# Optimization experiments

Hardware: AMD Instinct MI355X
Metric: run time of the kernel (lower is better)

Reference implementation:

```python
import jax, jax.numpy as jnp
import numpy as np

S_MC = 4      # num_mc_samples
TEMP = 0.1    # soft_sampling temperature


def gcn_conv(x, adj, maskf, W, b):
    # DenseGCNConv: add self loops, sym-normalize, aggregate, linear, mask
    N = adj.shape[-1]
    A = adj + jnp.eye(N, dtype=adj.dtype)
    dis = jnp.clip(A.sum(-1), 1.0, None) ** -0.5
    A = dis[:, :, None] * A * dis[:, None, :]
    out = jnp.einsum('bij,bjf->bif', A, x @ W) + b
    return out * maskf[:, :, None]


def connected_components(adj, mask):
    # min-label propagation; labels in {1..N}, masked nodes -> 0
    B, N, _ = adj.shape
    labels0 = jnp.broadcast_to(jnp.arange(1, N + 1, dtype=jnp.int32), (B, N))
    big = jnp.int32(N + 2)
    adj_b = adj > 0
    def step(labels, _):
        nb = jnp.where(adj_b, labels[:, None, :], big)  # [B,N,N]
        return jnp.minimum(labels, nb.min(-1)), None
    labels, _ = jax.lax.scan(step, labels0, None, length=N)
    return jnp.where(mask, labels, 0)


def setup_inputs() -> dict:
    key = jax.random.key(0)
    ks = jax.random.split(key, 8)
    B, N, Fin, H, K = 512, 64, 128, 256, 32
    x = jax.random.normal(ks[0], (B, N, Fin), jnp.float32)
    lengths = jax.random.randint(ks[1], (B,), N // 2, N + 1)
    mask = jnp.arange(N)[None, :] < lengths[:, None]
    a = jax.random.uniform(ks[2], (B, N, N)) < 0.08
    adj = jnp.triu(a, 1)
    adj = (adj | jnp.swapaxes(adj, 1, 2)).astype(jnp.float32)
    adj = adj * mask[:, :, None] * mask[:, None, :]
    W1 = jax.random.normal(ks[3], (Fin, H), jnp.float32) / np.float32(np.sqrt(Fin))
    b1 = jnp.zeros((H,), jnp.float32)
    W2 = jax.random.normal(ks[4], (H, H), jnp.float32) / np.float32(np.sqrt(H))
    b2 = jnp.zeros((H,), jnp.float32)
    centroids = jax.random.normal(ks[5], (K, H), jnp.float32)
    return {'x': x, 'adj': adj, 'mask': mask, 'W1': W1, 'b1': b1, 'W2': W2, 'b2': b2, 'centroids': centroids}


def reference(x, adj, mask, W1, b1, W2, b2, centroids):
    B, N = mask.shape
    maskf = mask.astype(x.dtype)
    adj = adj * maskf[:, :, None] * maskf[:, None, :]
    # embedding convs
    h = jax.nn.relu(gcn_conv(x, adj, maskf, W1, b1))
    h = jax.nn.relu(gcn_conv(h, adj, maskf, W2, b2))
    # cdist to (detached) centroids, expanded form to avoid [B,N,K,F] blowup
    c = jax.lax.stop_gradient(centroids)
    d2 = (jnp.sum(h * h, -1, keepdims=True) + jnp.sum(c * c, -1)[None, None]
          - 2.0 * jnp.einsum('bnf,kf->bnk', h, c))
    dist = jnp.sqrt(jnp.clip(d2, 1e-12, None))  # [B,N,K]
    # softmin over clusters with temperature
    logits = -dist / TEMP
    probs = jax.nn.softmax(logits, -1)
    logp = jax.nn.log_softmax(logits, -1)
    # Categorical MC sampling via Gumbel-max
    g = jax.random.gumbel(jax.random.key(42), (S_MC,) + logp.shape, logp.dtype)
    concepts = jnp.argmax(logp[None] + g, -1).reshape(S_MC * B, N)  # [SB,N]
    # per-node sampled probability, product over valid nodes per graph (scatter mul)
    probs_r = jnp.tile(probs, (S_MC, 1, 1))
    node_p = jnp.take_along_axis(probs_r, concepts[..., None], -1)[..., 0]
    mask_r = jnp.tile(mask, (S_MC, 1))
    graph_prob = jnp.prod(jnp.where(mask_r, jax.lax.stop_gradient(node_p), 1.0), -1)  # [SB]
    # same-concept restricted adjacency -> connected components (undirected)
    adj_r = jnp.tile(adj, (S_MC, 1, 1))
    same = concepts[:, :, None] == concepts[:, None, :]
    adj_cc = jnp.where(same, adj_r, 0.0)
    adj_cc = jnp.maximum(adj_cc, jnp.swapaxes(adj_cc, 1, 2))
    labels = connected_components(adj_cc, mask_r)  # [SB,N], 0 reserved for masked
    # scatter-mean node embeddings per cluster; drop reserved cluster 0
    P = jax.nn.one_hot(labels, N + 1, dtype=x.dtype) * mask_r[..., None].astype(x.dtype)  # [SB,N,N+1]
    counts = P.sum(1)  # [SB,N+1]
    h_r = jnp.tile(h, (S_MC, 1, 1))
    new_x = (jnp.einsum('bnc,bnf->bcf', P, h_r) / jnp.clip(counts, 1.0, None)[..., None])[:, 1:, :]
    # pooled adjacency S^T A S, binarized
    new_adj = jnp.einsum('bic,bij,bjd->bcd', P, adj_r, P)[:, 1:, 1:]
    new_adj = (new_adj > 0).astype(x.dtype)
    return new_x, new_adj, graph_prob, labels
```

## Files before the change

kernel.cpp:

```cpp
#include <hip/hip_runtime.h>

#define B_    512

static constexpr float TINYF = 1.17549435e-38f;
typedef float fx4  __attribute__((ext_vector_type(4)));
typedef short bf16x8 __attribute__((ext_vector_type(8)));
typedef float f32x4 __attribute__((ext_vector_type(4)));
typedef unsigned short u16x4 __attribute__((ext_vector_type(4)));

__device__ __forceinline__ float fmul_s(float a, float b) { float r; asm("v_mul_f32 %0, %1, %2" : "=v"(r) : "v"(a), "v"(b)); return r; }
__device__ __forceinline__ float fadd_s(float a, float b) { float r; asm("v_add_f32 %0, %1, %2" : "=v"(r) : "v"(a), "v"(b)); return r; }
__device__ __forceinline__ float fsub_s(float a, float b) { float r; asm("v_sub_f32 %0, %1, %2" : "=v"(r) : "v"(a), "v"(b)); return r; }

__device__ __forceinline__ unsigned tf_bits(unsigned lo) {
  const unsigned ks0 = 0u, ks1 = 42u, ks2 = 0x1BD11BF0u;
  unsigned x0 = 0u + ks0;
  unsigned x1 = lo + ks1;
#define TFR(r) { x0 += x1; x1 = (x1 << r) | (x1 >> (32 - r)); x1 ^= x0; }
  TFR(13) TFR(15) TFR(26) TFR(6)
  x0 += ks1; x1 += ks2 + 1u;
  TFR(17) TFR(29) TFR(16) TFR(24)
  x0 += ks2; x1 += ks0 + 2u;
  TFR(13) TFR(15) TFR(26) TFR(6)
  x0 += ks0; x1 += ks1 + 3u;
  TFR(17) TFR(29) TFR(16) TFR(24)
  x0 += ks1; x1 += ks2 + 4u;
  TFR(13) TFR(15) TFR(26) TFR(6)
  x0 += ks2; x1 += ks0 + 5u;
#undef TFR
  return x0 ^ x1;
}

__device__ __forceinline__ void split3(float v, unsigned& b1, unsigned& b2, unsigned& b3) {
  unsigned u1 = __float_as_uint(v) & 0xFFFF0000u;
  float r1 = v - __uint_as_float(u1);
  unsigned u2 = __float_as_uint(r1) & 0xFFFF0000u;
  float r2 = r1 - __uint_as_float(u2);
  unsigned u3 = __float_as_uint(r2) & 0xFFFF0000u;
  b1 = u1 >> 16; b2 = u2 >> 16; b3 = u3 >> 16;
}

__device__ __forceinline__ unsigned short planeOf(float v, int s) {
  unsigned u1 = __float_as_uint(v) & 0xFFFF0000u;
  if (s == 0) return (unsigned short)(u1 >> 16);
  float r1 = v - __uint_as_float(u1);
  unsigned u2 = __float_as_uint(r1) & 0xFFFF0000u;
  if (s == 1) return (unsigned short)(u2 >> 16);
  float r2 = r1 - __uint_as_float(u2);
  return (unsigned short)((__float_as_uint(r2) & 0xFFFF0000u) >> 16);
}

#define MF6(A0, A1, A2, Bv0, Bv1, Bv2, ACC)                                   \
  ACC = __builtin_amdgcn_mfma_f32_16x16x32_bf16(A0, Bv0, ACC, 0, 0, 0);       \
  ACC = __builtin_amdgcn_mfma_f32_16x16x32_bf16(A0, Bv1, ACC, 0, 0, 0);       \
  ACC = __builtin_amdgcn_mfma_f32_16x16x32_bf16(A1, Bv0, ACC, 0, 0, 0);       \
  ACC = __builtin_amdgcn_mfma_f32_16x16x32_bf16(A0, Bv2, ACC, 0, 0, 0);       \
  ACC = __builtin_amdgcn_mfma_f32_16x16x32_bf16(A1, Bv1, ACC, 0, 0, 0);       \
  ACC = __builtin_amdgcn_mfma_f32_16x16x32_bf16(A2, Bv0, ACC, 0, 0, 0);

__global__ void k_setup(const float* __restrict__ W1, const float* __restrict__ W2,
                        const float* __restrict__ cen,
                        unsigned short* __restrict__ Wg1, unsigned short* __restrict__ Wg2,
                        unsigned short* __restrict__ cen3, float* __restrict__ ccbuf) {
  int bi = blockIdx.x, tid = threadIdx.x;
  if (bi < 144) {
    const float* W; unsigned short* Wg; int nk, s, ks, g;
    if (bi < 48) { W = W1; Wg = Wg1; nk = 4; s = bi >> 4; ks = (bi >> 2) & 3; g = bi & 3; }
    else { int t = bi - 48; W = W2; Wg = Wg2; nk = 8; s = t >> 5; ks = (t >> 2) & 7; g = t & 3; }
    int n = tid;
    bf16x8 hv;
#pragma unroll
    for (int jj = 0; jj < 8; ++jj) {
      float v = W[(size_t)(ks * 32 + g * 8 + jj) * 256 + n];
      hv[jj] = (short)planeOf(v, s);
    }
    *(bf16x8*)&Wg[((((size_t)s * nk + ks) * 4 + g) * 256 + n) * 8] = hv;
  } else if (bi == 144) {
    int k = tid >> 3, l8 = tid & 7;
    float s = 0.0f;
    for (int m = 0; m < 32; ++m) { float v = cen[k * 256 + l8 + 8 * m]; s += v * v; }
#pragma unroll
    for (int d = 1; d < 8; d <<= 1) s += __shfl_xor(s, d, 64);
    if (l8 == 0) ccbuf[k] = s;
  } else {
    int s = bi - 145;
    for (int u = 0; u < 4; ++u) {
      int idx = tid + 256 * u;
      int ks = idx >> 7, c = (idx >> 6) & 1, rem = idx & 63;
      int l15v = rem >> 2, lgv = rem & 3;
      bf16x8 hv;
#pragma unroll
      for (int jj = 0; jj < 8; ++jj)
        hv[jj] = (short)planeOf(cen[(size_t)(16 * c + l15v) * 256 + 32 * ks + 8 * lgv + jj], s);
      *(bf16x8*)&cen3[(size_t)s * 8192 + (size_t)idx * 8] = hv;
    }
  }
}

__device__ __forceinline__ void layer_core(const float* __restrict__ A,
                                           const unsigned short* __restrict__ Wg,
                                           const unsigned short* AhP,
                                           const float* biaS, const float* maskS,
                                           float* __restrict__ out, int nk,
                                           char* U, int b, int tid) {
  unsigned short (*Ap)[3][2112] = (unsigned short(*)[3][2112])U;
  unsigned short (*Tbuf)[72]    = (unsigned short(*)[72])U;
  int w = tid >> 6, l = tid & 63;
  int l15 = l & 15, lg = l >> 4;
  int K = nk * 32;
  int srow = tid >> 2, sg = tid & 3;
  const float* sp = A + (size_t)srow * K + sg * 8;

  {
    float4 v0 = *(const float4*)(sp);
    float4 v1 = *(const float4*)(sp + 4);
    float vv[8] = {v0.x, v0.y, v0.z, v0.w, v1.x, v1.y, v1.z, v1.w};
    bf16x8 p1, p2, p3;
#pragma unroll
    for (int jj = 0; jj < 8; ++jj) {
      unsigned h1, h2, h3; split3(vv[jj], h1, h2, h3);
      p1[jj] = (short)h1; p2[jj] = (short)h2; p3[jj] = (short)h3;
    }
    int off = sg * 528 + srow * 8;
    *(bf16x8*)&Ap[0][0][off] = p1;
    *(bf16x8*)&Ap[0][1][off] = p2;
    *(bf16x8*)&Ap[0][2][off] = p3;
  }
  __syncthreads();

  f32x4 acc1[4][4];
#pragma unroll
  for (int q = 0; q < 4; ++q)
#pragma unroll
    for (int c = 0; c < 4; ++c) acc1[q][c] = (f32x4){0.f, 0.f, 0.f, 0.f};

  const size_t wss = (size_t)nk * 8192;

  for (int ks = 0; ks < nk; ++ks) {
    int cur = ks & 1;
    float4 v0, v1;
    bool pf = (ks + 1 < nk);
    if (pf) {
      v0 = *(const float4*)(sp + (ks + 1) * 32);
      v1 = *(const float4*)(sp + (ks + 1) * 32 + 4);
    }
    bf16x8 af[4][3];
#pragma unroll
    for (int q = 0; q < 4; ++q) {
      int off = lg * 528 + (16 * q + l15) * 8;
#pragma unroll
      for (int s = 0; s < 3; ++s) af[q][s] = *(const bf16x8*)&Ap[cur][s][off];
    }
#pragma unroll
    for (int c = 0; c < 4; ++c) {
      size_t wbase = (((size_t)ks * 4 + lg) * 256 + (64 * w + 16 * c + l15)) * 8;
      bf16x8 b0 = *(const bf16x8*)&Wg[wbase];
      bf16x8 b1 = *(const bf16x8*)&Wg[wbase + wss];
      bf16x8 b2 = *(const bf16x8*)&Wg[wbase + 2 * wss];
#pragma unroll
      for (int q = 0; q < 4; ++q) {
        MF6(af[q][0], af[q][1], af[q][2], b0, b1, b2, acc1[q][c]);
      }
    }
    if (pf) {
      float vv[8] = {v0.x, v0.y, v0.z, v0.w, v1.x, v1.y, v1.z, v1.w};
      bf16x8 p1, p2, p3;
#pragma unroll
      for (int jj = 0; jj < 8; ++jj) {
        unsigned h1, h2, h3; split3(vv[jj], h1, h2, h3);
        p1[jj] = (short)h1; p2[jj] = (short)h2; p3[jj] = (short)h3;
      }
      int off = sg * 528 + srow * 8;
      *(bf16x8*)&Ap[cur ^ 1][0][off] = p1;
      *(bf16x8*)&Ap[cur ^ 1][1][off] = p2;
      *(bf16x8*)&Ap[cur ^ 1][2][off] = p3;
    }
    __syncthreads();
  }

  f32x4 acc2[4][4];
#pragma unroll
  for (int q = 0; q < 4; ++q)
#pragma unroll
    for (int c = 0; c < 4; ++c) acc2[q][c] = (f32x4){0.f, 0.f, 0.f, 0.f};

#pragma unroll
  for (int sB = 0; sB < 3; ++sB) {
    const int nA = 3 - sB;
    __syncthreads();
#pragma unroll
    for (int q = 0; q < 4; ++q)
#pragma unroll
      for (int c = 0; c < 4; ++c) {
        u16x4 pv;
#pragma unroll
        for (int r = 0; r < 4; ++r) pv[r] = planeOf(acc1[q][c][r], sB);
        *(u16x4*)&Tbuf[64 * w + 16 * c + l15][16 * q + 4 * lg] = pv;
      }
    __syncthreads();
#pragma unroll
    for (int mt = 0; mt < 2; ++mt) {
      bf16x8 bf[4];
#pragma unroll
      for (int c = 0; c < 4; ++c)
        bf[c] = *(const bf16x8*)&Tbuf[64 * w + 16 * c + l15][32 * mt + 8 * lg];
#pragma unroll
      for (int q2 = 0; q2 < 4; ++q2) {
        bf16x8 afr[3];
#pragma unroll
        for (int sA = 0; sA < 3; ++sA)
          if (sA < nA)
            afr[sA] = *(const bf16x8*)&AhP[((((size_t)(sA * 2 + mt) * 4 + q2) * 4 + lg) * 16 + l15) * 8];
#pragma unroll
        for (int c = 0; c < 4; ++c)
#pragma unroll
          for (int sA = 0; sA < 3; ++sA)
            if (sA < nA)
              acc2[q2][c] = __builtin_amdgcn_mfma_f32_16x16x32_bf16(afr[sA], bf[c], acc2[q2][c], 0, 0, 0);
      }
    }
  }

#pragma unroll
  for (int q2 = 0; q2 < 4; ++q2) {
#pragma unroll
    for (int c = 0; c < 4; ++c) {
      int n = 64 * w + 16 * c + l15;
      float bv = biaS[n];
#pragma unroll
      for (int r = 0; r < 4; ++r) {
        int row = 16 * q2 + 4 * lg + r;
        float val = (acc2[q2][c][r] + bv) * maskS[row];
        out[((size_t)b * 64 + row) * 256 + n] = fmaxf(val, 0.0f);
      }
    }
  }
}

__global__ __launch_bounds__(256, 2) void k_fused(
    const float* __restrict__ x, const float* __restrict__ adj,
    const void* __restrict__ mp,
    const float* __restrict__ b1v, const float* __restrict__ b2v,
    const unsigned short* __restrict__ Wg1, const unsigned short* __restrict__ Wg2,
    unsigned long long* __restrict__ nbr, float* __restrict__ maskf,
    float* __restrict__ bufA, float* __restrict__ bufB) {
  __shared__ unsigned short AhP[12288];
  __shared__ float biaS[256];
  __shared__ float maskS[64];
  __shared__ int s_ni, s_nf;
  __shared__ __align__(16) char U[36864];

  int b = blockIdx.x, tid = threadIdx.x;

  {
    float* adjS = (float*)U;
    float (*AhS)[65] = (float(*)[65])(U + 16384);
    float* dis = (float*)(U + 33024);
    if (tid == 0) { s_ni = 0; s_nf = 0; }
    const float* ab = adj + (size_t)b * 4096;
    for (int i = tid; i < 4096; i += 256) adjS[i] = ab[i];
    {
      const unsigned* wp = (const unsigned*)mp;
      int ni = 0, nf = 0;
      for (int i = tid; i < 2048; i += 256) {
        unsigned v = wp[i];
        if (v > 1u) ni = 1;
        if (v != 0u && v != 0x3f800000u) nf = 1;
      }
      if (ni) atomicOr(&s_ni, 1);
      if (nf) atomicOr(&s_nf, 1);
    }
    biaS[tid] = b1v[tid];
    __syncthreads();
    if (tid < 64) {
      float s = 0.0f;
      unsigned long long m = 0ull;
      for (int j = 0; j < 64; ++j) {
        float v = adjS[j * 64 + tid];
        s += (j == tid) ? (v + 1.0f) : v;
        if (v != 0.0f) m |= (1ull << j);
      }
      dis[tid] = 1.0f / sqrtf(fmaxf(s, 1.0f));
      nbr[b * 64 + tid] = m;
      int fl = s_ni ? (s_nf ? 2 : 1) : 0;
      int i = b * 64 + tid;
      float r;
      if (fl == 0)      r = ((const int*)mp)[i] ? 1.0f : 0.0f;
      else if (fl == 1) r = (((const float*)mp)[i] != 0.0f) ? 1.0f : 0.0f;
      else              r = ((const unsigned char*)mp)[i] ? 1.0f : 0.0f;
      maskS[tid] = r;
      maskf[i] = r;
    }
    __syncthreads();
    for (int i = tid; i < 4096; i += 256) {
      int r = i >> 6, c = i & 63;
      float a = adjS[i] + ((r == c) ? 1.0f : 0.0f);
      AhS[r][c] = (dis[r] * a) * dis[c];
    }
    __syncthreads();
    for (int ch = tid; ch < 1536; ch += 256) {
      int l15v = ch & 15, lgv = (ch >> 4) & 3, q2 = (ch >> 6) & 3, mt = (ch >> 8) & 1, s = ch >> 9;
      bf16x8 hv;
#pragma unroll
      for (int jj = 0; jj < 8; ++jj)
        hv[jj] = (short)planeOf(AhS[16 * q2 + l15v][32 * mt + 8 * lgv + jj], s);
      *(bf16x8*)&AhP[(size_t)ch * 8] = hv;
    }
    __syncthreads();
  }

  layer_core(x + (size_t)b * 64 * 128, Wg1, AhP, biaS, maskS, bufA, 4, U, b, tid);
  __syncthreads();
  biaS[tid] = b2v[tid];

  layer_core(bufA + (size_t)b * 64 * 256, Wg2, AhP, biaS, maskS, bufB, 8, U, b, tid);
}

__global__ __launch_bounds__(256, 3) void k_cdsp(const float* __restrict__ h,
                                                 const unsigned short* __restrict__ cen3,
                                                 const float* __restrict__ ccbuf,
                                                 const float* __restrict__ maskf,
                                                 const unsigned long long* __restrict__ nbr,
                                                 float* __restrict__ out_newx,
                                                 float* __restrict__ out_newadj,
                                                 float* __restrict__ out_gp,
                                                 float* __restrict__ out_lab) {
  __shared__ float Dred[4][64][36];
  __shared__ float hhp[64][4];
  __shared__ float lgp[64][33];
  __shared__ float mxs[64], lgden[64];
  __shared__ int concS[4][64];
  __shared__ float ppS[4][64];
  __shared__ int labFS[4][64];

  int b = blockIdx.x, tid = threadIdx.x;
  int w = tid >> 6, l = tid & 63, l15 = l & 15, lg = l >> 4;
  const float* hb = h + (size_t)b * 16384;

  {
    int row = tid & 63, qt = tid >> 6;
    float s = 0.0f;
    for (int u = 0; u < 16; ++u) {
      float4 v = *(const float4*)&hb[row * 256 + qt * 64 + u * 4];
      float t = fadd_s(fadd_s(fadd_s(fmul_s(v.x, v.x), fmul_s(v.y, v.y)), fmul_s(v.z, v.z)), fmul_s(v.w, v.w));
      s = fadd_s(s, t);
    }
    hhp[row][qt] = s;
  }

  f32x4 acc[4][2];
#pragma unroll
  for (int qt = 0; qt < 4; ++qt)
#pragma unroll
    for (int c = 0; c < 2; ++c) acc[qt][c] = (f32x4){0.f, 0.f, 0.f, 0.f};

#pragma unroll
  for (int ks2 = 0; ks2 < 2; ++ks2) {
    int ks = 2 * w + ks2;
#pragma unroll
    for (int qt = 0; qt < 4; ++qt) {
      int row = 16 * qt + l15;
      float4 v0 = *(const float4*)&hb[row * 256 + 32 * ks + 8 * lg];
      float4 v1 = *(const float4*)&hb[row * 256 + 32 * ks + 8 * lg + 4];
      float vv[8] = {v0.x, v0.y, v0.z, v0.w, v1.x, v1.y, v1.z, v1.w};
      bf16x8 a0, a1, a2;
#pragma unroll
      for (int jj = 0; jj < 8; ++jj) {
        unsigned h1, h2, h3; split3(vv[jj], h1, h2, h3);
        a0[jj] = (short)h1; a1[jj] = (short)h2; a2[jj] = (short)h3;
      }
#pragma unroll
      for (int c = 0; c < 2; ++c) {
        const unsigned short* cb = cen3 + ((size_t)(ks * 2 + c) * 64 + l15 * 4 + lg) * 8;
        bf16x8 b0 = *(const bf16x8*)cb;
        bf16x8 b1 = *(const bf16x8*)(cb + 8192);
        bf16x8 b2 = *(const bf16x8*)(cb + 16384);
        MF6(a0, a1, a2, b0, b1, b2, acc[qt][c]);
      }
    }
  }

#pragma unroll
  for (int qt = 0; qt < 4; ++qt)
#pragma unroll
    for (int c = 0; c < 2; ++c)
#pragma unroll
      for (int r = 0; r < 4; ++r)
        Dred[w][16 * qt + 4 * lg + r][16 * c + l15] = acc[qt][c][r];
  __syncthreads();

  {
    int n = tid >> 2, kq = tid & 3;
    float hh = (hhp[n][0] + hhp[n][1]) + (hhp[n][2] + hhp[n][3]);
#pragma unroll
    for (int j = 0; j < 8; ++j) {
      int k = kq * 8 + j;
      float dot = (Dred[0][n][k] + Dred[1][n][k]) + (Dred[2][n][k] + Dred[3][n][k]);
      float d2 = fsub_s(fadd_s(hh, ccbuf[k]), fmul_s(2.0f, dot));
      lgp[n][k] = -10.0f * sqrtf(fmaxf(d2, 1e-12f));
    }
  }
  __syncthreads();

  if (tid < 64) {
    float mx = -1e30f;
    for (int k = 0; k < 32; ++k) mx = fmaxf(mx, lgp[tid][k]);
    float den = 0.0f;
    for (int k = 0; k < 32; ++k) den += expf(lgp[tid][k] - mx);
    mxs[tid] = mx; lgden[tid] = logf(den);
  }
  __syncthreads();
  for (int p = tid; p < 2048; p += 256) {
    int n = p >> 5, k = p & 31;
    lgp[n][k] = (lgp[n][k] - mxs[n]) - lgden[n];
  }
  __syncthreads();

  {
    int hw = tid >> 5, k = tid & 31;
    for (int pass = 0; pass < 8; ++pass) {
      int n = hw * 8 + pass;
      float lp = lgp[n][k];
#pragma unroll
      for (int s4 = 0; s4 < 4; ++s4) {
        unsigned flat = (unsigned)(s4 * 32768 + b * 64 + n) * 32u + (unsigned)k;
        unsigned bits = tf_bits(flat);
        float fu = __uint_as_float((bits >> 9) | 0x3f800000u) - 1.0f;
        float u = fmaxf(TINYF, fadd_s(fmul_s(fu, 1.0f - TINYF), TINYF));
        float g = -logf(-logf(u));
        float v = lp + g;
        int bi = k;
#pragma unroll
        for (int d = 1; d < 32; d <<= 1) {
          float ov = __shfl_xor(v, d, 32);
          int oi = __shfl_xor(bi, d, 32);
          if (ov > v || (ov == v && oi < bi)) { v = ov; bi = oi; }
        }
        if (k == 0) {
          concS[s4][n] = bi;
          ppS[s4][n] = expf(lgp[n][bi]);
        }
      }
    }
  }
  __syncthreads();

  {
    unsigned char (*o)[4096] = (unsigned char(*)[4096])Dred;
    int s = w, lane = l;
    int sbo = s * 512 + b;
    int c0 = concS[s][lane];
    bool mk = maskf[b * 64 + lane] != 0.0f;
    unsigned long long nb = nbr[b * 64 + lane];
    unsigned long long sm = 0ull;
    {
      unsigned long long t = nb;
      while (t) { int j = __ffsll(t) - 1; if (concS[s][j] == c0) sm |= (1ull << j); t &= t - 1; }
    }
    labFS[s][lane] = lane + 1;
    for (int it = 0; it < 64; ++it) {
      int m = labFS[s][lane];
      unsigned long long t = sm;
      while (t) { int j = __ffsll(t) - 1; m = min(m, labFS[s][j]); t &= t - 1; }
      bool ch = m < labFS[s][lane];
      if (ch) labFS[s][lane] = m;
      if (!__any(ch)) break;
    }
    int lf = mk ? labFS[s][lane] : 0;
    out_lab[(size_t)sbo * 64 + lane] = (float)lf;
    float pv = mk ? ppS[s][lane] : 1.0f;
#pragma unroll
    for (int d = 1; d < 64; d <<= 1) pv *= __shfl_xor(pv, d, 64);
    if (lane == 0) out_gp[sbo] = pv;
    labFS[s][lane] = lf;
    unsigned long long cm = 0ull;
    for (int j = 0; j < 64; ++j)
      if (labFS[s][j] == lane + 1) cm |= (1ull << j);
    {
      unsigned* op = (unsigned*)o[s];
#pragma unroll
      for (int u = 0; u < 16; ++u) op[u * 64 + lane] = 0u;
      if (lf > 0) {
        unsigned long long t = nb;
        while (t) {
          int j = __ffsll(t) - 1; t &= t - 1;
          int lj = labFS[s][j];
          if (lj > 0) o[s][(lf - 1) * 64 + (lj - 1)] = 1;
        }
      }
      float* dA = out_newadj + (size_t)sbo * 4096;
#pragma unroll
      for (int u = 0; u < 16; ++u) {
        int base = u * 256 + lane * 4;
        fx4 v;
        v.x = o[s][base + 0] ? 1.0f : 0.0f;
        v.y = o[s][base + 1] ? 1.0f : 0.0f;
        v.z = o[s][base + 2] ? 1.0f : 0.0f;
        v.w = o[s][base + 3] ? 1.0f : 0.0f;
        *(fx4*)&dA[base] = v;
      }
    }
    float* dX = out_newx + (size_t)sbo * 16384;
    for (int c = 0; c < 64; ++c) {
      unsigned long long m = __shfl(cm, c, 64);
      float4 acc4 = make_float4(0.f, 0.f, 0.f, 0.f);
      unsigned long long t = m;
      while (t) {
        int j = __ffsll(t) - 1; t &= t - 1;
        float4 v = *(const float4*)&hb[j * 256 + lane * 4];
        acc4.x += v.x; acc4.y += v.y; acc4.z += v.z; acc4.w += v.w;
      }
      int cnt = __popcll(m);
      float cf = (float)(cnt > 0 ? cnt : 1);
      fx4 r;
      r.x = acc4.x / cf; r.y = acc4.y / cf; r.z = acc4.z / cf; r.w = acc4.w / cf;
      *(fx4*)&dX[(size_t)c * 256 + lane * 4] = r;
    }
  }
}

extern "C" void kernel_launch(void* const* d_in, const int* in_sizes, int n_in,
                              void* d_out, int out_size, void* d_ws, size_t ws_size,
                              hipStream_t stream) {
  (void)in_sizes; (void)n_in; (void)out_size; (void)ws_size;
  const float* x   = (const float*)d_in[0];
  const float* adj = (const float*)d_in[1];
  const void*  mp  = d_in[2];
  const float* W1  = (const float*)d_in[3];
  const float* b1  = (const float*)d_in[4];
  const float* W2  = (const float*)d_in[5];
  const float* b2  = (const float*)d_in[6];
  const float* cen = (const float*)d_in[7];

  char* ws = (char*)d_ws;
  unsigned short* Wg1  = (unsigned short*)(ws + 0);
  unsigned short* Wg2  = (unsigned short*)(ws + 196608);
  unsigned short* cen3 = (unsigned short*)(ws + 589824);
  float* ccbuf         = (float*)(ws + 638976);
  unsigned long long* nbr = (unsigned long long*)(ws + 655360);
  float* maskf         = (float*)(ws + 917504);
  float* bufA          = (float*)(ws + 2097152);
  float* bufB          = (float*)(ws + 37748736);

  float* out        = (float*)d_out;
  float* out_newx   = out;
  float* out_newadj = out + 33554432;
  float* out_gp     = out + 41943040;
  float* out_lab    = out + 41945088;

  hipLaunchKernelGGL(k_setup, dim3(148), dim3(256), 0, stream, W1, W2, cen, Wg1, Wg2, cen3, ccbuf);
  hipLaunchKernelGGL(k_fused, dim3(512), dim3(256), 0, stream, x, adj, mp, b1, b2,
                     Wg1, Wg2, nbr, maskf, bufA, bufB);
  hipLaunchKernelGGL(k_cdsp,  dim3(512), dim3(256), 0, stream, bufB, cen3, ccbuf, maskf, nbr,
                     out_newx, out_newadj, out_gp, out_lab);
}
```

Baseline: 149.7 us.

## Split cdist/sampling and cluster pooling into separate kernels with per-wave rows

The fused cdist+sampling+pooling kernel is split in two. The first kernel gives each wave 16 node rows over the full K dimension, so there is no cross-wave reduction and no __syncthreads. It writes the sampled concepts and probabilities to workspace. A second kernel with 2048 single-wave blocks runs connected components, pooled adjacency and scatter-mean per sample, which gives finer-grained parallelism for the divergent pooling stage. This adds an extra launch and a round trip through global memory for concepts and probabilities.

```diff
diff --git a/kernel.cpp b/kernel.cpp
--- a/kernel.cpp
+++ b/kernel.cpp
@@ -316,52 +316,46 @@
   layer_core(bufA + (size_t)b * 64 * 256, Wg2, AhP, biaS, maskS, bufB, 8, U, b, tid);
 }
 
-__global__ __launch_bounds__(256, 3) void k_cdsp(const float* __restrict__ h,
-                                                 const unsigned short* __restrict__ cen3,
-                                                 const float* __restrict__ ccbuf,
-                                                 const float* __restrict__ maskf,
-                                                 const unsigned long long* __restrict__ nbr,
-                                                 float* __restrict__ out_newx,
-                                                 float* __restrict__ out_newadj,
-                                                 float* __restrict__ out_gp,
-                                                 float* __restrict__ out_lab) {
-  __shared__ float Dred[4][64][36];
-  __shared__ float hhp[64][4];
-  __shared__ float lgp[64][33];
-  __shared__ float mxs[64], lgden[64];
-  __shared__ int concS[4][64];
-  __shared__ float ppS[4][64];
-  __shared__ int labFS[4][64];
+__global__ __launch_bounds__(256, 4) void k_cd(const float* __restrict__ h,
+                                               const unsigned short* __restrict__ cen3,
+                                               const float* __restrict__ ccbuf,
+                                               int* __restrict__ conc,
+                                               float* __restrict__ pp) {
+  __shared__ float lgpS[4][16][33];
+  __shared__ float hhS[64];
+  __shared__ float mxS[64], ldS[64];
 
   int b = blockIdx.x, tid = threadIdx.x;
   int w = tid >> 6, l = tid & 63, l15 = l & 15, lg = l >> 4;
   const float* hb = h + (size_t)b * 16384;
 
   {
-    int row = tid & 63, qt = tid >> 6;
+    int row = 16 * w + (l >> 2), q = l & 3;
     float s = 0.0f;
     for (int u = 0; u < 16; ++u) {
-      float4 v = *(const float4*)&hb[row * 256 + qt * 64 + u * 4];
+      float4 v = *(const float4*)&hb[row * 256 + q * 64 + u * 4];
       float t = fadd_s(fadd_s(fadd_s(fmul_s(v.x, v.x), fmul_s(v.y, v.y)), fmul_s(v.z, v.z)), fmul_s(v.w, v.w));
       s = fadd_s(s, t);
     }
-    hhp[row][qt] = s;
-  }
-
-  f32x4 acc[4][2];
-#pragma unroll
-  for (int qt = 0; qt < 4; ++qt)
-#pragma unroll
-    for (int c = 0; c < 2; ++c) acc[qt][c] = (f32x4){0.f, 0.f, 0.f, 0.f};
-
-#pragma unroll
-  for (int ks2 = 0; ks2 < 2; ++ks2) {
-    int ks = 2 * w + ks2;
-#pragma unroll
-    for (int qt = 0; qt < 4; ++qt) {
-      int row = 16 * qt + l15;
-      float4 v0 = *(const float4*)&hb[row * 256 + 32 * ks + 8 * lg];
-      float4 v1 = *(const float4*)&hb[row * 256 + 32 * ks + 8 * lg + 4];
+    float s1 = fadd_s(s, __shfl_xor(s, 1, 64));
+    float s2 = fadd_s(s1, __shfl_xor(s1, 2, 64));
+    if (q == 0) hhS[row] = s2;
+  }
+
+  f32x4 accP[4][2];
+#pragma unroll
+  for (int p = 0; p < 4; ++p)
+#pragma unroll
+    for (int c = 0; c < 2; ++c) accP[p][c] = (f32x4){0.f, 0.f, 0.f, 0.f};
+
+  int arow = 16 * w + l15;
+#pragma unroll
+  for (int p = 0; p < 4; ++p) {
+#pragma unroll
+    for (int ks2 = 0; ks2 < 2; ++ks2) {
+      int ks = 2 * p + ks2;
+      float4 v0 = *(const float4*)&hb[arow * 256 + 32 * ks + 8 * lg];
+      float4 v1 = *(const float4*)&hb[arow * 256 + 32 * ks + 8 * lg + 4];
       float vv[8] = {v0.x, v0.y, v0.z, v0.w, v1.x, v1.y, v1.z, v1.w};
       bf16x8 a0, a1, a2;
 #pragma unroll
@@ -375,147 +369,149 @@
         bf16x8 b0 = *(const bf16x8*)cb;
         bf16x8 b1 = *(const bf16x8*)(cb + 8192);
         bf16x8 b2 = *(const bf16x8*)(cb + 16384);
-        MF6(a0, a1, a2, b0, b1, b2, acc[qt][c]);
-      }
-    }
-  }
-
-#pragma unroll
-  for (int qt = 0; qt < 4; ++qt)
-#pragma unroll
-    for (int c = 0; c < 2; ++c)
-#pragma unroll
-      for (int r = 0; r < 4; ++r)
-        Dred[w][16 * qt + 4 * lg + r][16 * c + l15] = acc[qt][c][r];
-  __syncthreads();
+        MF6(a0, a1, a2, b0, b1, b2, accP[p][c]);
+      }
+    }
+  }
+
+#pragma unroll
+  for (int c = 0; c < 2; ++c) {
+    int k = 16 * c + l15;
+    float cc = ccbuf[k];
+#pragma unroll
+    for (int r = 0; r < 4; ++r) {
+      int rr = 4 * lg + r;
+      float dotv = fadd_s(fadd_s(accP[0][c][r], accP[1][c][r]),
+                          fadd_s(accP[2][c][r], accP[3][c][r]));
+      float hh = hhS[16 * w + rr];
+      float d2 = fsub_s(fadd_s(hh, cc), fmul_s(2.0f, dotv));
+      lgpS[w][rr][k] = -10.0f * sqrtf(fmaxf(d2, 1e-12f));
+    }
+  }
+
+  if (l < 16) {
+    float mx = -1e30f;
+    for (int k = 0; k < 32; ++k) mx = fmaxf(mx, lgpS[w][l][k]);
+    float den = 0.0f;
+    for (int k = 0; k < 32; ++k) den += expf(lgpS[w][l][k] - mx);
+    mxS[16 * w + l] = mx; ldS[16 * w + l] = logf(den);
+  }
+  for (int p4 = l; p4 < 512; p4 += 64) {
+    int rr = p4 >> 5, k = p4 & 31;
+    lgpS[w][rr][k] = (lgpS[w][rr][k] - mxS[16 * w + rr]) - ldS[16 * w + rr];
+  }
 
   {
-    int n = tid >> 2, kq = tid & 3;
-    float hh = (hhp[n][0] + hhp[n][1]) + (hhp[n][2] + hhp[n][3]);
-#pragma unroll
-    for (int j = 0; j < 8; ++j) {
-      int k = kq * 8 + j;
-      float dot = (Dred[0][n][k] + Dred[1][n][k]) + (Dred[2][n][k] + Dred[3][n][k]);
-      float d2 = fsub_s(fadd_s(hh, ccbuf[k]), fmul_s(2.0f, dot));
-      lgp[n][k] = -10.0f * sqrtf(fmaxf(d2, 1e-12f));
-    }
-  }
-  __syncthreads();
-
-  if (tid < 64) {
-    float mx = -1e30f;
-    for (int k = 0; k < 32; ++k) mx = fmaxf(mx, lgp[tid][k]);
-    float den = 0.0f;
-    for (int k = 0; k < 32; ++k) den += expf(lgp[tid][k] - mx);
-    mxs[tid] = mx; lgden[tid] = logf(den);
-  }
-  __syncthreads();
-  for (int p = tid; p < 2048; p += 256) {
-    int n = p >> 5, k = p & 31;
-    lgp[n][k] = (lgp[n][k] - mxs[n]) - lgden[n];
-  }
-  __syncthreads();
-
+    int half = l >> 5, k = l & 31;
+    for (int u = 0; u < 32; ++u) {
+      int unit = 2 * u + half;
+      int rr = unit >> 2, s4 = unit & 3;
+      int node = 16 * w + rr;
+      float lp = lgpS[w][rr][k];
+      unsigned flat = (unsigned)(s4 * 32768 + b * 64 + node) * 32u + (unsigned)k;
+      unsigned bits = tf_bits(flat);
+      float fu = __uint_as_float((bits >> 9) | 0x3f800000u) - 1.0f;
+      float uu = fmaxf(TINYF, fadd_s(fmul_s(fu, 1.0f - TINYF), TINYF));
+      float g = -logf(-logf(uu));
+      float v = lp + g;
+      int bi = k;
+#pragma unroll
+      for (int d = 1; d < 32; d <<= 1) {
+        float ov = __shfl_xor(v, d, 32);
+        int oi = __shfl_xor(bi, d, 32);
+        if (ov > v || (ov == v && oi < bi)) { v = ov; bi = oi; }
+      }
+      if (k == 0) {
+        conc[s4 * 32768 + b * 64 + node] = bi;
+        pp[s4 * 32768 + b * 64 + node] = expf(lgpS[w][rr][bi]);
+      }
+    }
+  }
+}
+
+__global__ __launch_bounds__(64) void k_post(const int* __restrict__ conc,
+                                             const float* __restrict__ pp,
+                                             const float* __restrict__ maskf,
+                                             const unsigned long long* __restrict__ nbr,
+                                             const float* __restrict__ h,
+                                             float* __restrict__ out_newx,
+                                             float* __restrict__ out_newadj,
+                                             float* __restrict__ out_gp,
+                                             float* __restrict__ out_lab) {
+  __shared__ int cs[64];
+  __shared__ int labF[64];
+  __shared__ unsigned char o[4096];
+
+  int sb = blockIdx.x, b = sb & 511, lane = threadIdx.x;
+  const float* hb = h + (size_t)b * 16384;
+
+  int c0 = conc[sb * 64 + lane];
+  cs[lane] = c0;
+  bool mk = maskf[b * 64 + lane] != 0.0f;
+  unsigned long long nb = nbr[b * 64 + lane];
+  unsigned long long sm = 0ull;
   {
-    int hw = tid >> 5, k = tid & 31;
-    for (int pass = 0; pass < 8; ++pass) {
-      int n = hw * 8 + pass;
-      float lp = lgp[n][k];
-#pragma unroll
-      for (int s4 = 0; s4 < 4; ++s4) {
-        unsigned flat = (unsigned)(s4 * 32768 + b * 64 + n) * 32u + (unsigned)k;
-        unsigned bits = tf_bits(flat);
-        float fu = __uint_as_float((bits >> 9) | 0x3f800000u) - 1.0f;
-        float u = fmaxf(TINYF, fadd_s(fmul_s(fu, 1.0f - TINYF), TINYF));
-        float g = -logf(-logf(u));
-        float v = lp + g;
-        int bi = k;
-#pragma unroll
-        for (int d = 1; d < 32; d <<= 1) {
-          float ov = __shfl_xor(v, d, 32);
-          int oi = __shfl_xor(bi, d, 32);
-          if (ov > v || (ov == v && oi < bi)) { v = ov; bi = oi; }
-        }
-        if (k == 0) {
-          concS[s4][n] = bi;
-          ppS[s4][n] = expf(lgp[n][bi]);
-        }
-      }
-    }
-  }
-  __syncthreads();
-
+    unsigned long long t = nb;
+    while (t) { int j = __ffsll(t) - 1; if (cs[j] == c0) sm |= (1ull << j); t &= t - 1; }
+  }
+  labF[lane] = lane + 1;
+  for (int it = 0; it < 64; ++it) {
+    int m = labF[lane];
+    unsigned long long t = sm;
+    while (t) { int j = __ffsll(t) - 1; m = min(m, labF[j]); t &= t - 1; }
+    bool ch = m < labF[lane];
+    if (ch) labF[lane] = m;
+    if (!__any(ch)) break;
+  }
+  int lf = mk ? labF[lane] : 0;
+  out_lab[(size_t)sb * 64 + lane] = (float)lf;
+  float pv = mk ? pp[sb * 64 + lane] : 1.0f;
+#pragma unroll
+  for (int d = 1; d < 64; d <<= 1) pv *= __shfl_xor(pv, d, 64);
+  if (lane == 0) out_gp[sb] = pv;
+  labF[lane] = lf;
+  unsigned long long cm = 0ull;
+  for (int j = 0; j < 64; ++j)
+    if (labF[j] == lane + 1) cm |= (1ull << j);
   {
-    unsigned char (*o)[4096] = (unsigned char(*)[4096])Dred;
-    int s = w, lane = l;
-    int sbo = s * 512 + b;
-    int c0 = concS[s][lane];
-    bool mk = maskf[b * 64 + lane] != 0.0f;
-    unsigned long long nb = nbr[b * 64 + lane];
-    unsigned long long sm = 0ull;
-    {
+    unsigned* op = (unsigned*)o;
+#pragma unroll
+    for (int u = 0; u < 16; ++u) op[u * 64 + lane] = 0u;
+    if (lf > 0) {
       unsigned long long t = nb;
-      while (t) { int j = __ffsll(t) - 1; if (concS[s][j] == c0) sm |= (1ull << j); t &= t - 1; }
-    }
-    labFS[s][lane] = lane + 1;
-    for (int it = 0; it < 64; ++it) {
-      int m = labFS[s][lane];
-      unsigned long long t = sm;
-      while (t) { int j = __ffsll(t) - 1; m = min(m, labFS[s][j]); t &= t - 1; }
-      bool ch = m < labFS[s][lane];
-      if (ch) labFS[s][lane] = m;
-      if (!__any(ch)) break;
-    }
-    int lf = mk ? labFS[s][lane] : 0;
-    out_lab[(size_t)sbo * 64 + lane] = (float)lf;
-    float pv = mk ? ppS[s][lane] : 1.0f;
-#pragma unroll
-    for (int d = 1; d < 64; d <<= 1) pv *= __shfl_xor(pv, d, 64);
-    if (lane == 0) out_gp[sbo] = pv;
-    labFS[s][lane] = lf;
-    unsigned long long cm = 0ull;
-    for (int j = 0; j < 64; ++j)
-      if (labFS[s][j] == lane + 1) cm |= (1ull << j);
-    {
-      unsigned* op = (unsigned*)o[s];
-#pragma unroll
-      for (int u = 0; u < 16; ++u) op[u * 64 + lane] = 0u;
-      if (lf > 0) {
-        unsigned long long t = nb;
-        while (t) {
-          int j = __ffsll(t) - 1; t &= t - 1;
-          int lj = labFS[s][j];
-          if (lj > 0) o[s][(lf - 1) * 64 + (lj - 1)] = 1;
-        }
-      }
-      float* dA = out_newadj + (size_t)sbo * 4096;
-#pragma unroll
-      for (int u = 0; u < 16; ++u) {
-        int base = u * 256 + lane * 4;
-        fx4 v;
-        v.x = o[s][base + 0] ? 1.0f : 0.0f;
-        v.y = o[s][base + 1] ? 1.0f : 0.0f;
-        v.z = o[s][base + 2] ? 1.0f : 0.0f;
-        v.w = o[s][base + 3] ? 1.0f : 0.0f;
-        *(fx4*)&dA[base] = v;
-      }
-    }
-    float* dX = out_newx + (size_t)sbo * 16384;
-    for (int c = 0; c < 64; ++c) {
-      unsigned long long m = __shfl(cm, c, 64);
-      float4 acc4 = make_float4(0.f, 0.f, 0.f, 0.f);
-      unsigned long long t = m;
       while (t) {
         int j = __ffsll(t) - 1; t &= t - 1;
-        float4 v = *(const float4*)&hb[j * 256 + lane * 4];
-        acc4.x += v.x; acc4.y += v.y; acc4.z += v.z; acc4.w += v.w;
-      }
-      int cnt = __popcll(m);
-      float cf = (float)(cnt > 0 ? cnt : 1);
-      fx4 r;
-      r.x = acc4.x / cf; r.y = acc4.y / cf; r.z = acc4.z / cf; r.w = acc4.w / cf;
-      *(fx4*)&dX[(size_t)c * 256 + lane * 4] = r;
-    }
+        int lj = labF[j];
+        if (lj > 0) o[(lf - 1) * 64 + (lj - 1)] = 1;
+      }
+    }
+    float* dA = out_newadj + (size_t)sb * 4096;
+#pragma unroll
+    for (int u = 0; u < 16; ++u) {
+      int base = u * 256 + lane * 4;
+      fx4 v;
+      v.x = o[base + 0] ? 1.0f : 0.0f;
+      v.y = o[base + 1] ? 1.0f : 0.0f;
+      v.z = o[base + 2] ? 1.0f : 0.0f;
+      v.w = o[base + 3] ? 1.0f : 0.0f;
+      *(fx4*)&dA[base] = v;
+    }
+  }
+  float* dX = out_newx + (size_t)sb * 16384;
+  for (int c = 0; c < 64; ++c) {
+    unsigned long long m = __shfl(cm, c, 64);
+    float4 acc4 = make_float4(0.f, 0.f, 0.f, 0.f);
+    unsigned long long t = m;
+    while (t) {
+      int j = __ffsll(t) - 1; t &= t - 1;
+      float4 v = *(const float4*)&hb[j * 256 + lane * 4];
+      acc4.x += v.x; acc4.y += v.y; acc4.z += v.z; acc4.w += v.w;
+    }
+    int cnt = __popcll(m);
+    float cf = (float)(cnt > 0 ? cnt : 1);
+    fx4 r;
+    r.x = acc4.x / cf; r.y = acc4.y / cf; r.z = acc4.z / cf; r.w = acc4.w / cf;
+    *(fx4*)&dX[(size_t)c * 256 + lane * 4] = r;
   }
 }
 
@@ -539,6 +535,8 @@
   float* ccbuf         = (float*)(ws + 638976);
   unsigned long long* nbr = (unsigned long long*)(ws + 655360);
   float* maskf         = (float*)(ws + 917504);
+  int*   conc          = (int*)(ws + 1048576);
+  float* pp            = (float*)(ws + 1572864);
   float* bufA          = (float*)(ws + 2097152);
   float* bufB          = (float*)(ws + 37748736);
 
@@ -551,6 +549,7 @@
   hipLaunchKernelGGL(k_setup, dim3(148), dim3(256), 0, stream, W1, W2, cen, Wg1, Wg2, cen3, ccbuf);
   hipLaunchKernelGGL(k_fused, dim3(512), dim3(256), 0, stream, x, adj, mp, b1, b2,
                      Wg1, Wg2, nbr, maskf, bufA, bufB);
-  hipLaunchKernelGGL(k_cdsp,  dim3(512), dim3(256), 0, stream, bufB, cen3, ccbuf, maskf, nbr,
+  hipLaunchKernelGGL(k_cd,    dim3(512), dim3(256), 0, stream, bufB, cen3, ccbuf, conc, pp);
+  hipLaunchKernelGGL(k_post,  dim3(2048), dim3(64), 0, stream, conc, pp, maskf, nbr, bufB,
                      out_newx, out_newadj, out_gp, out_lab);
 }
```

Result: slower. 154.0 us (+2.8%).
